# Performance work log

Measured on AMD Instinct MI355X. Metric: run time of the kernel, lower is better.

Reference implementation:

```python
import jax, jax.numpy as jnp
import numpy as np

EMBED_DIM = 1024
NUM_HEADS = 16
HEAD_DIM = EMBED_DIM // NUM_HEADS
B, N = 8, 1024


def setup_inputs() -> dict:
    key = jax.random.key(0)
    k1, k2, k3, k4, k5, k6 = jax.random.split(key, 6)
    scale = 1.0 / np.sqrt(EMBED_DIM)
    return {
        "x": jax.random.normal(k1, (B, N, EMBED_DIM), dtype=jnp.float32),
        "attn_mask": jax.random.normal(k2, (N, N), dtype=jnp.float32) * 0.1,
        "in_proj_weight": jax.random.normal(k3, (3 * EMBED_DIM, EMBED_DIM), dtype=jnp.float32) * scale,
        "in_proj_bias": jax.random.normal(k4, (3 * EMBED_DIM,), dtype=jnp.float32) * 0.02,
        "out_w": jax.random.normal(k5, (EMBED_DIM, EMBED_DIM), dtype=jnp.float32) * scale,
        "out_b": jax.random.normal(k6, (EMBED_DIM,), dtype=jnp.float32) * 0.02,
    }


def reference(x, attn_mask, in_proj_weight, in_proj_bias, out_w, out_b):
    # x: (B, N, C); fused QKV projection as in forward_direct
    Bn, Nn, C = x.shape
    H, D = NUM_HEADS, HEAD_DIM
    qkv = x @ in_proj_weight.T + in_proj_bias            # (B, N, 3C)
    qkv = qkv.reshape(Bn, Nn, 3, H, D).transpose(2, 0, 3, 1, 4)  # (3, B, H, N, D)
    q, k, v = qkv[0], qkv[1], qkv[2]
    q = q / jnp.sqrt(jnp.asarray(D, dtype=q.dtype))
    attn = jnp.einsum("bhnd,bhmd->bhnm", q, k)           # (B, H, N, N) scores
    attn = attn + attn_mask                              # broadcast over (B, H)
    attn = jax.nn.softmax(attn, axis=-1)
    out = jnp.einsum("bhnm,bhmd->bhnd", attn, v)         # (B, H, N, D)
    out = out.transpose(0, 2, 1, 3).reshape(Bn, Nn, C)   # (B, N, C)
    return out @ out_w.T + out_b
```

## Files before the change

### kernel.cpp

```cpp
#include <hip/hip_runtime.h>


typedef __bf16 bf16x8 __attribute__((ext_vector_type(8)));
typedef float f32x4 __attribute__((ext_vector_type(4)));
typedef unsigned short us4v __attribute__((ext_vector_type(4)));

#define MFMA16 __builtin_amdgcn_mfma_f32_16x16x32_bf16

__device__ __forceinline__ unsigned short f2bf(float f) {
    return __builtin_bit_cast(unsigned short, (__bf16)f);
}

__device__ __forceinline__ us4v cvt4(float4 v) {
    us4v r;
    r.x = f2bf(v.x); r.y = f2bf(v.y); r.z = f2bf(v.z); r.w = f2bf(v.w);
    return r;
}

__device__ __forceinline__ void gl16(const unsigned short* g, unsigned short* l) {
    __builtin_amdgcn_global_load_lds(
        (const __attribute__((address_space(1))) unsigned*)g,
        (__attribute__((address_space(3))) unsigned*)l, 16, 0, 0);
}

__global__ __launch_bounds__(256)
void cvt_bf16(const float* __restrict__ src, unsigned short* __restrict__ dst,
              int n4) {
    const int i = blockIdx.x * 256 + threadIdx.x;
    if (i < n4) {
        float4 v = ((const float4*)src)[i];
        ((us4v*)dst)[i] = cvt4(v);
    }
}

__global__ __launch_bounds__(256, 3)
void qkv_gemm(const unsigned short* __restrict__ xb,
              const unsigned short* __restrict__ wb,
              const float* __restrict__ bias,
              unsigned short* __restrict__ qb, unsigned short* __restrict__ kb,
              unsigned short* __restrict__ vbT)
{
    __shared__ unsigned short lsa[3][128 * 32];
    __shared__ unsigned short lsb[3][128 * 32];
    const int tid  = threadIdx.x;
    const int wave = tid >> 6, lane = tid & 63;
    const int quad = lane >> 4, l15 = lane & 15;
    const int rch = (quad ^ ((l15 >> 1) & 3)) * 8;
    const int m0 = blockIdx.x * 128, n0 = blockIdx.y * 128;
    const int wm = (wave & 1) * 64, wn = (wave >> 1) * 64;

    const int srow = wave * 32 + (lane >> 2);
    const int scol = ((lane & 3) ^ ((lane >> 3) & 3)) * 8;
    const unsigned short* ga = xb + (size_t)(m0 + srow) * 1024 + scol;
    const unsigned short* gb = wb + (size_t)(n0 + srow) * 1024 + scol;
    const int so0 = (wave * 32) * 32;
    const int so1 = (wave * 32 + 16) * 32;

    f32x4 acc[4][4];
#pragma unroll
    for (int i = 0; i < 4; ++i)
#pragma unroll
        for (int j = 0; j < 4; ++j) acc[i][j] = (f32x4){0.f, 0.f, 0.f, 0.f};

    gl16(ga, &lsa[0][so0]);
    gl16(ga + 16 * 1024, &lsa[0][so1]);
    gl16(gb, &lsb[0][so0]);
    gl16(gb + 16 * 1024, &lsb[0][so1]);
    gl16(ga + 32, &lsa[1][so0]);
    gl16(ga + 16 * 1024 + 32, &lsa[1][so1]);
    gl16(gb + 32, &lsb[1][so0]);
    gl16(gb + 16 * 1024 + 32, &lsb[1][so1]);

    for (int kt = 0; kt < 32; ++kt) {
        const int cb = kt % 3;
        if (kt < 30) {
            const int k0 = (kt + 2) * 32;
            const int sb = (kt + 2) % 3;
            gl16(ga + k0, &lsa[sb][so0]);
            gl16(ga + 16 * 1024 + k0, &lsa[sb][so1]);
            gl16(gb + k0, &lsb[sb][so0]);
            gl16(gb + 16 * 1024 + k0, &lsb[sb][so1]);
            asm volatile("s_waitcnt vmcnt(8)" ::: "memory");
        } else if (kt == 30) {
            asm volatile("s_waitcnt vmcnt(4)" ::: "memory");
        } else {
            asm volatile("s_waitcnt vmcnt(0)" ::: "memory");
        }
        __builtin_amdgcn_s_barrier();

        const unsigned short* pa = lsa[cb];
        const unsigned short* pb = lsb[cb];
        bf16x8 af[4], bfr[4];
#pragma unroll
        for (int i = 0; i < 4; ++i)
            af[i] = *(const bf16x8*)&pa[(wm + i * 16 + l15) * 32 + rch];
#pragma unroll
        for (int j = 0; j < 4; ++j)
            bfr[j] = *(const bf16x8*)&pb[(wn + j * 16 + l15) * 32 + rch];
#pragma unroll
        for (int i = 0; i < 4; ++i)
#pragma unroll
            for (int j = 0; j < 4; ++j)
                acc[i][j] = MFMA16(af[i], bfr[j], acc[i][j], 0, 0, 0);

        asm volatile("s_waitcnt lgkmcnt(0)" ::: "memory");
        __builtin_amdgcn_sched_barrier(0);
        __builtin_amdgcn_s_barrier();
    }

    const int which = n0 >> 10;
    if (which == 2) {
#pragma unroll
        for (int j = 0; j < 4; ++j) {
            const int n = n0 + wn + j * 16 + l15;
            const int c = n & 1023;
            const int h = c >> 6, d = c & 63;
            const float bv = bias[n];
#pragma unroll
            for (int i = 0; i < 4; ++i) {
                const int m = m0 + wm + i * 16 + quad * 4;
                const int b = m >> 10, s = m & 1023;
                us4v pk;
#pragma unroll
                for (int r = 0; r < 4; ++r) pk[r] = f2bf(acc[i][j][r] + bv);
                *(us4v*)&vbT[(size_t)((b * 16 + h) * 64 + d) * 1024 + s] = pk;
            }
        }
    } else {
        unsigned short* __restrict__ dst = (which == 0) ? qb : kb;
        const float sc = (which == 0) ? 0.125f : 1.0f;
#pragma unroll
        for (int j = 0; j < 4; ++j) {
            const int n = n0 + wn + j * 16 + l15;
            const int c = n & 1023;
            const int h = c >> 6, d = c & 63;
            const float bv = bias[n];
#pragma unroll
            for (int i = 0; i < 4; ++i)
#pragma unroll
                for (int r = 0; r < 4; ++r) {
                    const int m = m0 + wm + i * 16 + quad * 4 + r;
                    const int b = m >> 10, s = m & 1023;
                    const float v = (acc[i][j][r] + bv) * sc;
                    dst[(size_t)((b * 16 + h) * 1024 + s) * 64 + d] = f2bf(v);
                }
        }
    }
}

__global__ __launch_bounds__(256, 3)
void attn_kernel(const unsigned short* __restrict__ qb,
                 const unsigned short* __restrict__ kb,
                 const unsigned short* __restrict__ vbT,
                 const float* __restrict__ mask,
                 unsigned short* __restrict__ ob)
{
    __shared__ unsigned short lsk[2][2][64 * 32];
    __shared__ unsigned short lsv[2][2][64 * 32];
    __shared__ unsigned short lsp[4][2][16 * 64];
    const int tid  = threadIdx.x;
    const int wave = tid >> 6, lane = tid & 63;
    const int quad = lane >> 4, l15 = lane & 15;
    const int rch = (quad ^ ((l15 >> 1) & 3)) * 8;
    const int swz = (l15 & 7) << 3;
    const int p  = blockIdx.x;
    const int lg = (p & 7) * 128 + (p >> 3);
    const int bh = lg >> 3;
    const int q0 = (lg & 7) * 128;
    const int b = bh >> 4, h = bh & 15;

    const unsigned short* __restrict__ kbase = kb + (size_t)bh * 65536;
    const unsigned short* __restrict__ vtb  = vbT + (size_t)bh * 65536;

    const int scol = ((lane & 3) ^ ((lane >> 3) & 3)) * 8;
    const unsigned short* gk = kbase + (size_t)(wave * 16 + (lane >> 2)) * 64
                                     + scol;
    const unsigned short* gv = vtb + (size_t)(wave * 16 + (lane >> 2)) * 1024
                                   + scol;
    const int so = (wave * 16) * 32;

    bf16x8 bq[2][2];
#pragma unroll
    for (int g = 0; g < 2; ++g) {
        const unsigned short* qrow =
            qb + (size_t)(bh * 1024 + q0 + wave * 32 + g * 16 + l15) * 64;
        bq[g][0] = *(const bf16x8*)(qrow + quad * 8);
        bq[g][1] = *(const bf16x8*)(qrow + 32 + quad * 8);
    }

    float lsum[2] = {0.f, 0.f};
    f32x4 oacc[2][4];
#pragma unroll
    for (int g = 0; g < 2; ++g)
#pragma unroll
        for (int nt = 0; nt < 4; ++nt) oacc[g][nt] = (f32x4){0.f, 0.f, 0.f, 0.f};

    const float* __restrict__ mrow0 =
        mask + (size_t)(q0 + wave * 32 + l15) * 1024;
    const float* __restrict__ mrow1 = mrow0 + 16 * 1024;

    gl16(gk, &lsk[0][0][so]);
    gl16(gk + 32, &lsk[0][1][so]);
    gl16(gv, &lsv[0][0][so]);
    gl16(gv + 32, &lsv[0][1][so]);
    float4 mcur[2][4];
#pragma unroll
    for (int nt = 0; nt < 4; ++nt) {
        mcur[0][nt] = *(const float4*)&mrow0[nt * 16 + quad * 4];
        mcur[1][nt] = *(const float4*)&mrow1[nt * 16 + quad * 4];
    }
    __syncthreads();

    int buf = 0;
    for (int kt = 0; kt < 16; ++kt) {
        float4 mnext[2][4];
        if (kt < 15) {
            gl16(gk + (size_t)(kt + 1) * 4096, &lsk[buf ^ 1][0][so]);
            gl16(gk + (size_t)(kt + 1) * 4096 + 32, &lsk[buf ^ 1][1][so]);
            gl16(gv + (size_t)(kt + 1) * 64, &lsv[buf ^ 1][0][so]);
            gl16(gv + (size_t)(kt + 1) * 64 + 32, &lsv[buf ^ 1][1][so]);
            __builtin_amdgcn_sched_barrier(0);
#pragma unroll
            for (int nt = 0; nt < 4; ++nt) {
                mnext[0][nt] =
                    *(const float4*)&mrow0[(kt + 1) * 64 + nt * 16 + quad * 4];
                mnext[1][nt] =
                    *(const float4*)&mrow1[(kt + 1) * 64 + nt * 16 + quad * 4];
            }
        }

        const unsigned short* rk0 = lsk[buf][0];
        const unsigned short* rk1 = lsk[buf][1];
        f32x4 s[2][4];
        __builtin_amdgcn_s_setprio(1);
#pragma unroll
        for (int nt = 0; nt < 4; ++nt) {
            const bf16x8 k0 = *(const bf16x8*)&rk0[(nt * 16 + l15) * 32 + rch];
            const bf16x8 k1 = *(const bf16x8*)&rk1[(nt * 16 + l15) * 32 + rch];
            s[0][nt] = MFMA16(k0, bq[0][0], (f32x4){0.f, 0.f, 0.f, 0.f}, 0, 0, 0);
            s[0][nt] = MFMA16(k1, bq[0][1], s[0][nt], 0, 0, 0);
            s[1][nt] = MFMA16(k0, bq[1][0], (f32x4){0.f, 0.f, 0.f, 0.f}, 0, 0, 0);
            s[1][nt] = MFMA16(k1, bq[1][1], s[1][nt], 0, 0, 0);
        }
        __builtin_amdgcn_s_setprio(0);

        unsigned short* lp0 = lsp[wave][0];
        unsigned short* lp1 = lsp[wave][1];
#pragma unroll
        for (int nt = 0; nt < 4; ++nt) {
            us4v pk0, pk1;
#pragma unroll
            for (int r = 0; r < 4; ++r) {
                const float pe0 =
                    __expf(s[0][nt][r] + ((const float*)&mcur[0][nt])[r]);
                const float pe1 =
                    __expf(s[1][nt][r] + ((const float*)&mcur[1][nt])[r]);
                lsum[0] += pe0;
                lsum[1] += pe1;
                pk0[r] = f2bf(pe0);
                pk1[r] = f2bf(pe1);
            }
            const int off = (nt * 16 + quad * 4) ^ swz;
            *(us4v*)&lp0[(l15 << 6) + off] = pk0;
            *(us4v*)&lp1[(l15 << 6) + off] = pk1;
        }
        bf16x8 pb0[2], pb1[2];
        pb0[0] = *(const bf16x8*)&lp0[(l15 << 6) + ((quad * 8) ^ swz)];
        pb0[1] = *(const bf16x8*)&lp0[(l15 << 6) + ((32 + quad * 8) ^ swz)];
        pb1[0] = *(const bf16x8*)&lp1[(l15 << 6) + ((quad * 8) ^ swz)];
        pb1[1] = *(const bf16x8*)&lp1[(l15 << 6) + ((32 + quad * 8) ^ swz)];

        const unsigned short* rv0 = lsv[buf][0];
        const unsigned short* rv1 = lsv[buf][1];
        __builtin_amdgcn_s_setprio(1);
#pragma unroll
        for (int nt = 0; nt < 4; ++nt) {
            const bf16x8 v0 = *(const bf16x8*)&rv0[(nt * 16 + l15) * 32 + rch];
            const bf16x8 v1 = *(const bf16x8*)&rv1[(nt * 16 + l15) * 32 + rch];
            oacc[0][nt] = MFMA16(v0, pb0[0], oacc[0][nt], 0, 0, 0);
            oacc[0][nt] = MFMA16(v1, pb0[1], oacc[0][nt], 0, 0, 0);
            oacc[1][nt] = MFMA16(v0, pb1[0], oacc[1][nt], 0, 0, 0);
            oacc[1][nt] = MFMA16(v1, pb1[1], oacc[1][nt], 0, 0, 0);
        }
        __builtin_amdgcn_s_setprio(0);

        if (kt < 15) {
            asm volatile("s_waitcnt lgkmcnt(0)" ::: "memory");
            __builtin_amdgcn_sched_barrier(0);
            asm volatile("s_waitcnt vmcnt(8)" ::: "memory");
            __builtin_amdgcn_s_barrier();
#pragma unroll
            for (int g = 0; g < 2; ++g)
#pragma unroll
                for (int nt = 0; nt < 4; ++nt) mcur[g][nt] = mnext[g][nt];
        }
        buf ^= 1;
    }

#pragma unroll
    for (int g = 0; g < 2; ++g) {
        lsum[g] += __shfl_xor(lsum[g], 16, 64);
        lsum[g] += __shfl_xor(lsum[g], 32, 64);
    }
#pragma unroll
    for (int g = 0; g < 2; ++g) {
        const float inv = 1.0f / lsum[g];
        unsigned short* orow =
            ob + (size_t)(b * 1024 + q0 + wave * 32 + g * 16 + l15) * 1024
               + h * 64;
#pragma unroll
        for (int nt = 0; nt < 4; ++nt) {
            us4v o;
#pragma unroll
            for (int r = 0; r < 4; ++r) o[r] = f2bf(oacc[g][nt][r] * inv);
            *(us4v*)&orow[nt * 16 + quad * 4] = o;
        }
    }
}

__global__ __launch_bounds__(256, 3)
void out_gemm(const unsigned short* __restrict__ a,
              const unsigned short* __restrict__ wb,
              const float* __restrict__ bias, float* __restrict__ out)
{
    __shared__ unsigned short lsa[3][128 * 32];
    __shared__ unsigned short lsb[3][128 * 32];
    const int tid  = threadIdx.x;
    const int wave = tid >> 6, lane = tid & 63;
    const int quad = lane >> 4, l15 = lane & 15;
    const int rch = (quad ^ ((l15 >> 1) & 3)) * 8;
    const int m0 = blockIdx.x * 128, n0 = blockIdx.y * 128;
    const int wm = (wave & 1) * 64, wn = (wave >> 1) * 64;

    const int srow = wave * 32 + (lane >> 2);
    const int scol = ((lane & 3) ^ ((lane >> 3) & 3)) * 8;
    const unsigned short* ga = a + (size_t)(m0 + srow) * 1024 + scol;
    const unsigned short* gb = wb + (size_t)(n0 + srow) * 1024 + scol;
    const int so0 = (wave * 32) * 32;
    const int so1 = (wave * 32 + 16) * 32;

    f32x4 acc[4][4];
#pragma unroll
    for (int i = 0; i < 4; ++i)
#pragma unroll
        for (int j = 0; j < 4; ++j) acc[i][j] = (f32x4){0.f, 0.f, 0.f, 0.f};

    gl16(ga, &lsa[0][so0]);
    gl16(ga + 16 * 1024, &lsa[0][so1]);
    gl16(gb, &lsb[0][so0]);
    gl16(gb + 16 * 1024, &lsb[0][so1]);
    gl16(ga + 32, &lsa[1][so0]);
    gl16(ga + 16 * 1024 + 32, &lsa[1][so1]);
    gl16(gb + 32, &lsb[1][so0]);
    gl16(gb + 16 * 1024 + 32, &lsb[1][so1]);

    for (int kt = 0; kt < 32; ++kt) {
        const int cb = kt % 3;
        if (kt < 30) {
            const int k0 = (kt + 2) * 32;
            const int sb = (kt + 2) % 3;
            gl16(ga + k0, &lsa[sb][so0]);
            gl16(ga + 16 * 1024 + k0, &lsa[sb][so1]);
            gl16(gb + k0, &lsb[sb][so0]);
            gl16(gb + 16 * 1024 + k0, &lsb[sb][so1]);
            asm volatile("s_waitcnt vmcnt(8)" ::: "memory");
        } else if (kt == 30) {
            asm volatile("s_waitcnt vmcnt(4)" ::: "memory");
        } else {
            asm volatile("s_waitcnt vmcnt(0)" ::: "memory");
        }
        __builtin_amdgcn_s_barrier();

        const unsigned short* pa = lsa[cb];
        const unsigned short* pb = lsb[cb];
        bf16x8 af[4], bfr[4];
#pragma unroll
        for (int i = 0; i < 4; ++i)
            af[i] = *(const bf16x8*)&pa[(wm + i * 16 + l15) * 32 + rch];
#pragma unroll
        for (int j = 0; j < 4; ++j)
            bfr[j] = *(const bf16x8*)&pb[(wn + j * 16 + l15) * 32 + rch];
#pragma unroll
        for (int i = 0; i < 4; ++i)
#pragma unroll
            for (int j = 0; j < 4; ++j)
                acc[i][j] = MFMA16(af[i], bfr[j], acc[i][j], 0, 0, 0);

        asm volatile("s_waitcnt lgkmcnt(0)" ::: "memory");
        __builtin_amdgcn_sched_barrier(0);
        __builtin_amdgcn_s_barrier();
    }

#pragma unroll
    for (int j = 0; j < 4; ++j) {
        const int n = n0 + wn + j * 16 + l15;
        const float bv = bias[n];
#pragma unroll
        for (int i = 0; i < 4; ++i)
#pragma unroll
            for (int r = 0; r < 4; ++r) {
                const int m = m0 + wm + i * 16 + quad * 4 + r;
                out[(size_t)m * 1024 + n] = acc[i][j][r] + bv;
            }
    }
}

extern "C" void kernel_launch(void* const* d_in, const int* in_sizes, int n_in,
                              void* d_out, int out_size, void* d_ws, size_t ws_size,
                              hipStream_t stream) {
    const float* x    = (const float*)d_in[0];
    const float* mask = (const float*)d_in[1];
    const float* win  = (const float*)d_in[2];
    const float* bin  = (const float*)d_in[3];
    const float* wout = (const float*)d_in[4];
    const float* bout = (const float*)d_in[5];
    float* out = (float*)d_out;

    char* ws = (char*)d_ws;
    unsigned short* xb = (unsigned short*)(ws);
    unsigned short* ob = (unsigned short*)(ws);
    unsigned short* qb = (unsigned short*)(ws + (size_t)(16 << 20));
    unsigned short* kb = (unsigned short*)(ws + (size_t)(32 << 20));
    unsigned short* vbT = (unsigned short*)(ws + (size_t)(48 << 20));
    unsigned short* winb  = (unsigned short*)d_out;
    unsigned short* woutb = qb;

    cvt_bf16<<<dim3(8192), 256, 0, stream>>>(x, xb, 8 * 1024 * 1024 / 4);
    cvt_bf16<<<dim3(3072), 256, 0, stream>>>(win, winb, 3 * 1024 * 1024 / 4);
    qkv_gemm<<<dim3(64, 24), 256, 0, stream>>>(xb, winb, bin, qb, kb, vbT);
    attn_kernel<<<dim3(1024), 256, 0, stream>>>(qb, kb, vbT, mask, ob);
    cvt_bf16<<<dim3(1024), 256, 0, stream>>>(wout, woutb, 1024 * 1024 / 4);
    out_gemm<<<dim3(64, 8), 256, 0, stream>>>(ob, woutb, bout, out);
}
```

Before: 277.3 us.

## Load K/V fragments directly from global memory, dropping LDS staging and barriers

The attention kernel stops staging K and V tiles in shared memory through double-buffered global_load_lds with block barriers. Each wave now loads its own K and V MFMA fragments straight from global memory into registers every iteration, and the mask prefetch pipeline is removed. This cuts LDS use and all block-level synchronisation, which may raise occupancy. In exchange, every wave re-reads the same K/V data through the cache, and there is no software prefetch to hide global load latency.

```diff
diff --git a/kernel.cpp b/kernel.cpp
--- a/kernel.cpp
+++ b/kernel.cpp
@@ -155,13 +155,10 @@
                  const float* __restrict__ mask,
                  unsigned short* __restrict__ ob)
 {
-    __shared__ unsigned short lsk[2][2][64 * 32];
-    __shared__ unsigned short lsv[2][2][64 * 32];
     __shared__ unsigned short lsp[4][2][16 * 64];
     const int tid  = threadIdx.x;
     const int wave = tid >> 6, lane = tid & 63;
     const int quad = lane >> 4, l15 = lane & 15;
-    const int rch = (quad ^ ((l15 >> 1) & 3)) * 8;
     const int swz = (l15 & 7) << 3;
     const int p  = blockIdx.x;
     const int lg = (p & 7) * 128 + (p >> 3);
@@ -169,15 +166,10 @@
     const int q0 = (lg & 7) * 128;
     const int b = bh >> 4, h = bh & 15;
 
-    const unsigned short* __restrict__ kbase = kb + (size_t)bh * 65536;
-    const unsigned short* __restrict__ vtb  = vbT + (size_t)bh * 65536;
-
-    const int scol = ((lane & 3) ^ ((lane >> 3) & 3)) * 8;
-    const unsigned short* gk = kbase + (size_t)(wave * 16 + (lane >> 2)) * 64
-                                     + scol;
-    const unsigned short* gv = vtb + (size_t)(wave * 16 + (lane >> 2)) * 1024
-                                   + scol;
-    const int so = (wave * 16) * 32;
+    const unsigned short* gk =
+        kb + (size_t)bh * 65536 + (size_t)l15 * 64 + quad * 8;
+    const unsigned short* gv =
+        vbT + (size_t)bh * 65536 + (size_t)l15 * 1024 + quad * 8;
 
     bf16x8 bq[2][2];
 #pragma unroll
@@ -198,63 +190,53 @@
     const float* __restrict__ mrow0 =
         mask + (size_t)(q0 + wave * 32 + l15) * 1024;
     const float* __restrict__ mrow1 = mrow0 + 16 * 1024;
-
-    gl16(gk, &lsk[0][0][so]);
-    gl16(gk + 32, &lsk[0][1][so]);
-    gl16(gv, &lsv[0][0][so]);
-    gl16(gv + 32, &lsv[0][1][so]);
-    float4 mcur[2][4];
-#pragma unroll
-    for (int nt = 0; nt < 4; ++nt) {
-        mcur[0][nt] = *(const float4*)&mrow0[nt * 16 + quad * 4];
-        mcur[1][nt] = *(const float4*)&mrow1[nt * 16 + quad * 4];
-    }
-    __syncthreads();
-
-    int buf = 0;
+    unsigned short* lp0 = lsp[wave][0];
+    unsigned short* lp1 = lsp[wave][1];
+
     for (int kt = 0; kt < 16; ++kt) {
-        float4 mnext[2][4];
-        if (kt < 15) {
-            gl16(gk + (size_t)(kt + 1) * 4096, &lsk[buf ^ 1][0][so]);
-            gl16(gk + (size_t)(kt + 1) * 4096 + 32, &lsk[buf ^ 1][1][so]);
-            gl16(gv + (size_t)(kt + 1) * 64, &lsv[buf ^ 1][0][so]);
-            gl16(gv + (size_t)(kt + 1) * 64 + 32, &lsv[buf ^ 1][1][so]);
-            __builtin_amdgcn_sched_barrier(0);
-#pragma unroll
-            for (int nt = 0; nt < 4; ++nt) {
-                mnext[0][nt] =
-                    *(const float4*)&mrow0[(kt + 1) * 64 + nt * 16 + quad * 4];
-                mnext[1][nt] =
-                    *(const float4*)&mrow1[(kt + 1) * 64 + nt * 16 + quad * 4];
-            }
-        }
-
-        const unsigned short* rk0 = lsk[buf][0];
-        const unsigned short* rk1 = lsk[buf][1];
+        bf16x8 kf[4][2];
+#pragma unroll
+        for (int nt = 0; nt < 4; ++nt) {
+            const unsigned short* kr = gk + (size_t)(kt * 64 + nt * 16) * 64;
+            kf[nt][0] = *(const bf16x8*)(kr);
+            kf[nt][1] = *(const bf16x8*)(kr + 32);
+        }
+        float4 mv[2][4];
+#pragma unroll
+        for (int nt = 0; nt < 4; ++nt) {
+            mv[0][nt] = *(const float4*)&mrow0[kt * 64 + nt * 16 + quad * 4];
+            mv[1][nt] = *(const float4*)&mrow1[kt * 64 + nt * 16 + quad * 4];
+        }
+        bf16x8 vf[4][2];
+#pragma unroll
+        for (int nt = 0; nt < 4; ++nt) {
+            const unsigned short* vr = gv + (size_t)nt * 16 * 1024 + kt * 64;
+            vf[nt][0] = *(const bf16x8*)(vr);
+            vf[nt][1] = *(const bf16x8*)(vr + 32);
+        }
+
         f32x4 s[2][4];
         __builtin_amdgcn_s_setprio(1);
 #pragma unroll
         for (int nt = 0; nt < 4; ++nt) {
-            const bf16x8 k0 = *(const bf16x8*)&rk0[(nt * 16 + l15) * 32 + rch];
-            const bf16x8 k1 = *(const bf16x8*)&rk1[(nt * 16 + l15) * 32 + rch];
-            s[0][nt] = MFMA16(k0, bq[0][0], (f32x4){0.f, 0.f, 0.f, 0.f}, 0, 0, 0);
-            s[0][nt] = MFMA16(k1, bq[0][1], s[0][nt], 0, 0, 0);
-            s[1][nt] = MFMA16(k0, bq[1][0], (f32x4){0.f, 0.f, 0.f, 0.f}, 0, 0, 0);
-            s[1][nt] = MFMA16(k1, bq[1][1], s[1][nt], 0, 0, 0);
+            s[0][nt] = MFMA16(kf[nt][0], bq[0][0],
+                              (f32x4){0.f, 0.f, 0.f, 0.f}, 0, 0, 0);
+            s[0][nt] = MFMA16(kf[nt][1], bq[0][1], s[0][nt], 0, 0, 0);
+            s[1][nt] = MFMA16(kf[nt][0], bq[1][0],
+                              (f32x4){0.f, 0.f, 0.f, 0.f}, 0, 0, 0);
+            s[1][nt] = MFMA16(kf[nt][1], bq[1][1], s[1][nt], 0, 0, 0);
         }
         __builtin_amdgcn_s_setprio(0);
 
-        unsigned short* lp0 = lsp[wave][0];
-        unsigned short* lp1 = lsp[wave][1];
 #pragma unroll
         for (int nt = 0; nt < 4; ++nt) {
             us4v pk0, pk1;
 #pragma unroll
             for (int r = 0; r < 4; ++r) {
                 const float pe0 =
-                    __expf(s[0][nt][r] + ((const float*)&mcur[0][nt])[r]);
+                    __expf(s[0][nt][r] + ((const float*)&mv[0][nt])[r]);
                 const float pe1 =
-                    __expf(s[1][nt][r] + ((const float*)&mcur[1][nt])[r]);
+                    __expf(s[1][nt][r] + ((const float*)&mv[1][nt])[r]);
                 lsum[0] += pe0;
                 lsum[1] += pe1;
                 pk0[r] = f2bf(pe0);
@@ -270,31 +252,15 @@
         pb1[0] = *(const bf16x8*)&lp1[(l15 << 6) + ((quad * 8) ^ swz)];
         pb1[1] = *(const bf16x8*)&lp1[(l15 << 6) + ((32 + quad * 8) ^ swz)];
 
-        const unsigned short* rv0 = lsv[buf][0];
-        const unsigned short* rv1 = lsv[buf][1];
         __builtin_amdgcn_s_setprio(1);
 #pragma unroll
         for (int nt = 0; nt < 4; ++nt) {
-            const bf16x8 v0 = *(const bf16x8*)&rv0[(nt * 16 + l15) * 32 + rch];
-            const bf16x8 v1 = *(const bf16x8*)&rv1[(nt * 16 + l15) * 32 + rch];
-            oacc[0][nt] = MFMA16(v0, pb0[0], oacc[0][nt], 0, 0, 0);
-            oacc[0][nt] = MFMA16(v1, pb0[1], oacc[0][nt], 0, 0, 0);
-            oacc[1][nt] = MFMA16(v0, pb1[0], oacc[1][nt], 0, 0, 0);
-            oacc[1][nt] = MFMA16(v1, pb1[1], oacc[1][nt], 0, 0, 0);
+            oacc[0][nt] = MFMA16(vf[nt][0], pb0[0], oacc[0][nt], 0, 0, 0);
+            oacc[0][nt] = MFMA16(vf[nt][1], pb0[1], oacc[0][nt], 0, 0, 0);
+            oacc[1][nt] = MFMA16(vf[nt][0], pb1[0], oacc[1][nt], 0, 0, 0);
+            oacc[1][nt] = MFMA16(vf[nt][1], pb1[1], oacc[1][nt], 0, 0, 0);
         }
         __builtin_amdgcn_s_setprio(0);
-
-        if (kt < 15) {
-            asm volatile("s_waitcnt lgkmcnt(0)" ::: "memory");
-            __builtin_amdgcn_sched_barrier(0);
-            asm volatile("s_waitcnt vmcnt(8)" ::: "memory");
-            __builtin_amdgcn_s_barrier();
-#pragma unroll
-            for (int g = 0; g < 2; ++g)
-#pragma unroll
-                for (int nt = 0; nt < 4; ++nt) mcur[g][nt] = mnext[g][nt];
-        }
-        buf ^= 1;
     }
 
 #pragma unroll
```

Measured after the change: 363.8 us. +31.2%, slower.

## Rewrite attention with 32x32 MFMA, register-resident P, and exp2 softmax

Applied to the files above, without the earlier changes.

Rebuilds the attention inner loop around 32x32x16 bf16 MFMA so each wave owns 32 query rows. The probability tile is repacked in registers with cvt_pk_bf16 and permlane32_swap, which removes the LDS round-trip for P. Q and the mask are pre-scaled by log2(e) so exp2 replaces expf, and the mask is loaded straight into the MFMA accumulator as its initial value. This adds a small mask-scaling kernel and a full __syncthreads per tile, and drops the cross-iteration mask prefetch, so mask load latency is less hidden.

```diff
diff --git a/kernel.cpp b/kernel.cpp
--- a/kernel.cpp
+++ b/kernel.cpp
@@ -3,9 +3,12 @@
 
 typedef __bf16 bf16x8 __attribute__((ext_vector_type(8)));
 typedef float f32x4 __attribute__((ext_vector_type(4)));
+typedef float f32x16 __attribute__((ext_vector_type(16)));
 typedef unsigned short us4v __attribute__((ext_vector_type(4)));
+typedef unsigned int u32x4 __attribute__((ext_vector_type(4)));
 
 #define MFMA16 __builtin_amdgcn_mfma_f32_16x16x32_bf16
+#define MFMA32 __builtin_amdgcn_mfma_f32_32x32x16_bf16
 
 __device__ __forceinline__ unsigned short f2bf(float f) {
     return __builtin_bit_cast(unsigned short, (__bf16)f);
@@ -14,6 +17,12 @@
 __device__ __forceinline__ us4v cvt4(float4 v) {
     us4v r;
     r.x = f2bf(v.x); r.y = f2bf(v.y); r.z = f2bf(v.z); r.w = f2bf(v.w);
+    return r;
+}
+
+__device__ __forceinline__ unsigned cvtpk(float lo, float hi) {
+    unsigned r;
+    asm volatile("v_cvt_pk_bf16_f32 %0, %1, %2" : "=v"(r) : "v"(lo), "v"(hi));
     return r;
 }
 
@@ -30,6 +39,17 @@
     if (i < n4) {
         float4 v = ((const float4*)src)[i];
         ((us4v*)dst)[i] = cvt4(v);
+    }
+}
+
+__global__ __launch_bounds__(256)
+void scale_f32(const float* __restrict__ src, float* __restrict__ dst, int n4) {
+    const int i = blockIdx.x * 256 + threadIdx.x;
+    if (i < n4) {
+        float4 v = ((const float4*)src)[i];
+        const float s = 1.4426950408889634f;
+        v.x *= s; v.y *= s; v.z *= s; v.w *= s;
+        ((float4*)dst)[i] = v;
     }
 }
 
@@ -128,7 +148,7 @@
         }
     } else {
         unsigned short* __restrict__ dst = (which == 0) ? qb : kb;
-        const float sc = (which == 0) ? 0.125f : 1.0f;
+        const float sc = (which == 0) ? 0.18033688011112442f : 1.0f;
 #pragma unroll
         for (int j = 0; j < 4; ++j) {
             const int n = n0 + wn + j * 16 + l15;
@@ -152,170 +172,152 @@
 void attn_kernel(const unsigned short* __restrict__ qb,
                  const unsigned short* __restrict__ kb,
                  const unsigned short* __restrict__ vbT,
-                 const float* __restrict__ mask,
+                 const float* __restrict__ mask2,
                  unsigned short* __restrict__ ob)
 {
     __shared__ unsigned short lsk[2][2][64 * 32];
     __shared__ unsigned short lsv[2][2][64 * 32];
-    __shared__ unsigned short lsp[4][2][16 * 64];
     const int tid  = threadIdx.x;
     const int wave = tid >> 6, lane = tid & 63;
-    const int quad = lane >> 4, l15 = lane & 15;
-    const int rch = (quad ^ ((l15 >> 1) & 3)) * 8;
-    const int swz = (l15 & 7) << 3;
+    const int r5 = lane & 31, hl = lane >> 5;
+    const int rs = ((r5 >> 1) ^ (r5 >> 3)) & 3;
     const int p  = blockIdx.x;
     const int lg = (p & 7) * 128 + (p >> 3);
     const int bh = lg >> 3;
     const int q0 = (lg & 7) * 128;
-    const int b = bh >> 4, h = bh & 15;
+    const int b = bh >> 4, head = bh & 15;
 
     const unsigned short* __restrict__ kbase = kb + (size_t)bh * 65536;
     const unsigned short* __restrict__ vtb  = vbT + (size_t)bh * 65536;
 
-    const int scol = ((lane & 3) ^ ((lane >> 3) & 3)) * 8;
+    const int scol =
+        ((lane & 3) ^ ((lane >> 3) & 3) ^ ((2 * wave + (lane >> 5)) & 3)) * 8;
     const unsigned short* gk = kbase + (size_t)(wave * 16 + (lane >> 2)) * 64
                                      + scol;
     const unsigned short* gv = vtb + (size_t)(wave * 16 + (lane >> 2)) * 1024
                                    + scol;
     const int so = (wave * 16) * 32;
 
-    bf16x8 bq[2][2];
-#pragma unroll
-    for (int g = 0; g < 2; ++g) {
-        const unsigned short* qrow =
-            qb + (size_t)(bh * 1024 + q0 + wave * 32 + g * 16 + l15) * 64;
-        bq[g][0] = *(const bf16x8*)(qrow + quad * 8);
-        bq[g][1] = *(const bf16x8*)(qrow + 32 + quad * 8);
-    }
-
-    float lsum[2] = {0.f, 0.f};
-    f32x4 oacc[2][4];
-#pragma unroll
-    for (int g = 0; g < 2; ++g)
-#pragma unroll
-        for (int nt = 0; nt < 4; ++nt) oacc[g][nt] = (f32x4){0.f, 0.f, 0.f, 0.f};
-
-    const float* __restrict__ mrow0 =
-        mask + (size_t)(q0 + wave * 32 + l15) * 1024;
-    const float* __restrict__ mrow1 = mrow0 + 16 * 1024;
+    const int q = q0 + wave * 32 + r5;
+    bf16x8 bq[4];
+    {
+        const unsigned short* qrow = qb + (size_t)(bh * 1024 + q) * 64;
+#pragma unroll
+        for (int kk = 0; kk < 4; ++kk)
+            bq[kk] = *(const bf16x8*)(qrow + kk * 16 + hl * 8);
+    }
+
+    float lsum = 0.f;
+    f32x16 acc[2];
+#pragma unroll
+    for (int dt = 0; dt < 2; ++dt)
+#pragma unroll
+        for (int r = 0; r < 16; ++r) acc[dt][r] = 0.f;
+
+    const float* __restrict__ mq = mask2 + (size_t)q * 1024;
 
     gl16(gk, &lsk[0][0][so]);
     gl16(gk + 32, &lsk[0][1][so]);
     gl16(gv, &lsv[0][0][so]);
     gl16(gv + 32, &lsv[0][1][so]);
-    float4 mcur[2][4];
-#pragma unroll
-    for (int nt = 0; nt < 4; ++nt) {
-        mcur[0][nt] = *(const float4*)&mrow0[nt * 16 + quad * 4];
-        mcur[1][nt] = *(const float4*)&mrow1[nt * 16 + quad * 4];
-    }
     __syncthreads();
 
     int buf = 0;
     for (int kt = 0; kt < 16; ++kt) {
-        float4 mnext[2][4];
+        f32x16 msk[2];
+#pragma unroll
+        for (int t32 = 0; t32 < 2; ++t32)
+#pragma unroll
+            for (int oct = 0; oct < 4; ++oct) {
+                const float4 mv = *(const float4*)
+                    &mq[kt * 64 + t32 * 32 + oct * 8 + hl * 4];
+                msk[t32][4 * oct + 0] = mv.x;
+                msk[t32][4 * oct + 1] = mv.y;
+                msk[t32][4 * oct + 2] = mv.z;
+                msk[t32][4 * oct + 3] = mv.w;
+            }
+        __builtin_amdgcn_sched_barrier(0);
         if (kt < 15) {
             gl16(gk + (size_t)(kt + 1) * 4096, &lsk[buf ^ 1][0][so]);
             gl16(gk + (size_t)(kt + 1) * 4096 + 32, &lsk[buf ^ 1][1][so]);
             gl16(gv + (size_t)(kt + 1) * 64, &lsv[buf ^ 1][0][so]);
             gl16(gv + (size_t)(kt + 1) * 64 + 32, &lsv[buf ^ 1][1][so]);
-            __builtin_amdgcn_sched_barrier(0);
-#pragma unroll
-            for (int nt = 0; nt < 4; ++nt) {
-                mnext[0][nt] =
-                    *(const float4*)&mrow0[(kt + 1) * 64 + nt * 16 + quad * 4];
-                mnext[1][nt] =
-                    *(const float4*)&mrow1[(kt + 1) * 64 + nt * 16 + quad * 4];
-            }
-        }
-
-        const unsigned short* rk0 = lsk[buf][0];
-        const unsigned short* rk1 = lsk[buf][1];
-        f32x4 s[2][4];
-        __builtin_amdgcn_s_setprio(1);
-#pragma unroll
-        for (int nt = 0; nt < 4; ++nt) {
-            const bf16x8 k0 = *(const bf16x8*)&rk0[(nt * 16 + l15) * 32 + rch];
-            const bf16x8 k1 = *(const bf16x8*)&rk1[(nt * 16 + l15) * 32 + rch];
-            s[0][nt] = MFMA16(k0, bq[0][0], (f32x4){0.f, 0.f, 0.f, 0.f}, 0, 0, 0);
-            s[0][nt] = MFMA16(k1, bq[0][1], s[0][nt], 0, 0, 0);
-            s[1][nt] = MFMA16(k0, bq[1][0], (f32x4){0.f, 0.f, 0.f, 0.f}, 0, 0, 0);
-            s[1][nt] = MFMA16(k1, bq[1][1], s[1][nt], 0, 0, 0);
-        }
-        __builtin_amdgcn_s_setprio(0);
-
-        unsigned short* lp0 = lsp[wave][0];
-        unsigned short* lp1 = lsp[wave][1];
-#pragma unroll
-        for (int nt = 0; nt < 4; ++nt) {
-            us4v pk0, pk1;
-#pragma unroll
-            for (int r = 0; r < 4; ++r) {
-                const float pe0 =
-                    __expf(s[0][nt][r] + ((const float*)&mcur[0][nt])[r]);
-                const float pe1 =
-                    __expf(s[1][nt][r] + ((const float*)&mcur[1][nt])[r]);
-                lsum[0] += pe0;
-                lsum[1] += pe1;
-                pk0[r] = f2bf(pe0);
-                pk1[r] = f2bf(pe1);
-            }
-            const int off = (nt * 16 + quad * 4) ^ swz;
-            *(us4v*)&lp0[(l15 << 6) + off] = pk0;
-            *(us4v*)&lp1[(l15 << 6) + off] = pk1;
-        }
-        bf16x8 pb0[2], pb1[2];
-        pb0[0] = *(const bf16x8*)&lp0[(l15 << 6) + ((quad * 8) ^ swz)];
-        pb0[1] = *(const bf16x8*)&lp0[(l15 << 6) + ((32 + quad * 8) ^ swz)];
-        pb1[0] = *(const bf16x8*)&lp1[(l15 << 6) + ((quad * 8) ^ swz)];
-        pb1[1] = *(const bf16x8*)&lp1[(l15 << 6) + ((32 + quad * 8) ^ swz)];
-
-        const unsigned short* rv0 = lsv[buf][0];
-        const unsigned short* rv1 = lsv[buf][1];
-        __builtin_amdgcn_s_setprio(1);
-#pragma unroll
-        for (int nt = 0; nt < 4; ++nt) {
-            const bf16x8 v0 = *(const bf16x8*)&rv0[(nt * 16 + l15) * 32 + rch];
-            const bf16x8 v1 = *(const bf16x8*)&rv1[(nt * 16 + l15) * 32 + rch];
-            oacc[0][nt] = MFMA16(v0, pb0[0], oacc[0][nt], 0, 0, 0);
-            oacc[0][nt] = MFMA16(v1, pb0[1], oacc[0][nt], 0, 0, 0);
-            oacc[1][nt] = MFMA16(v0, pb1[0], oacc[1][nt], 0, 0, 0);
-            oacc[1][nt] = MFMA16(v1, pb1[1], oacc[1][nt], 0, 0, 0);
-        }
-        __builtin_amdgcn_s_setprio(0);
-
-        if (kt < 15) {
-            asm volatile("s_waitcnt lgkmcnt(0)" ::: "memory");
-            __builtin_amdgcn_sched_barrier(0);
-            asm volatile("s_waitcnt vmcnt(8)" ::: "memory");
-            __builtin_amdgcn_s_barrier();
-#pragma unroll
-            for (int g = 0; g < 2; ++g)
-#pragma unroll
-                for (int nt = 0; nt < 4; ++nt) mcur[g][nt] = mnext[g][nt];
-        }
+        }
+
+#pragma unroll
+        for (int t32 = 0; t32 < 2; ++t32) {
+            f32x16 s = msk[t32];
+            __builtin_amdgcn_s_setprio(1);
+#pragma unroll
+            for (int kk = 0; kk < 4; ++kk) {
+                const unsigned short* kp = lsk[buf][kk >> 1];
+                const int c4 = 2 * (kk & 1) + hl;
+                const bf16x8 ka = *(const bf16x8*)
+                    &kp[(t32 * 32 + r5) * 32 + ((c4 ^ rs) * 8)];
+                s = MFMA32(ka, bq[kk], s, 0, 0, 0);
+            }
+            __builtin_amdgcn_s_setprio(0);
+
+            float pv[16];
+            float ts = 0.f;
+#pragma unroll
+            for (int r = 0; r < 16; ++r) {
+                pv[r] = exp2f(s[r]);
+                ts += pv[r];
+            }
+            lsum += ts;
+
+            bf16x8 pfr[2];
+#pragma unroll
+            for (int cl = 0; cl < 2; ++cl) {
+                unsigned xa = cvtpk(pv[8 * cl + 0], pv[8 * cl + 1]);
+                unsigned xb = cvtpk(pv[8 * cl + 2], pv[8 * cl + 3]);
+                unsigned ya = cvtpk(pv[8 * cl + 4], pv[8 * cl + 5]);
+                unsigned yb = cvtpk(pv[8 * cl + 6], pv[8 * cl + 7]);
+                asm volatile("v_permlane32_swap_b32 %0, %1"
+                             : "+v"(xa), "+v"(ya));
+                asm volatile("v_permlane32_swap_b32 %0, %1"
+                             : "+v"(xb), "+v"(yb));
+                const u32x4 t = {xa, xb, ya, yb};
+                pfr[cl] = __builtin_bit_cast(bf16x8, t);
+            }
+
+            __builtin_amdgcn_s_setprio(1);
+#pragma unroll
+            for (int cl = 0; cl < 2; ++cl) {
+                const int cg = t32 * 2 + cl;
+                const unsigned short* vp = lsv[buf][cg >> 1];
+                const int c4v = 2 * (cg & 1) + hl;
+                const int voff = (c4v ^ rs) * 8;
+#pragma unroll
+                for (int dt = 0; dt < 2; ++dt) {
+                    const bf16x8 va = *(const bf16x8*)
+                        &vp[(dt * 32 + r5) * 32 + voff];
+                    acc[dt] = MFMA32(va, pfr[cl], acc[dt], 0, 0, 0);
+                }
+            }
+            __builtin_amdgcn_s_setprio(0);
+        }
+
+        __syncthreads();
         buf ^= 1;
     }
 
-#pragma unroll
-    for (int g = 0; g < 2; ++g) {
-        lsum[g] += __shfl_xor(lsum[g], 16, 64);
-        lsum[g] += __shfl_xor(lsum[g], 32, 64);
-    }
-#pragma unroll
-    for (int g = 0; g < 2; ++g) {
-        const float inv = 1.0f / lsum[g];
-        unsigned short* orow =
-            ob + (size_t)(b * 1024 + q0 + wave * 32 + g * 16 + l15) * 1024
-               + h * 64;
-#pragma unroll
-        for (int nt = 0; nt < 4; ++nt) {
+    lsum += __shfl_xor(lsum, 32, 64);
+    const float inv = 1.0f / lsum;
+
+    unsigned short* orow =
+        ob + (size_t)(b * 1024 + q) * 1024 + head * 64;
+#pragma unroll
+    for (int dt = 0; dt < 2; ++dt)
+#pragma unroll
+        for (int oct = 0; oct < 4; ++oct) {
             us4v o;
 #pragma unroll
-            for (int r = 0; r < 4; ++r) o[r] = f2bf(oacc[g][nt][r] * inv);
-            *(us4v*)&orow[nt * 16 + quad * 4] = o;
-        }
-    }
+            for (int r = 0; r < 4; ++r)
+                o[r] = f2bf(acc[dt][4 * oct + r] * inv);
+            *(us4v*)&orow[dt * 32 + oct * 8 + hl * 4] = o;
+        }
 }
 
 __global__ __launch_bounds__(256, 3)
@@ -423,12 +425,14 @@
     unsigned short* kb = (unsigned short*)(ws + (size_t)(32 << 20));
     unsigned short* vbT = (unsigned short*)(ws + (size_t)(48 << 20));
     unsigned short* winb  = (unsigned short*)d_out;
+    float* mask2 = (float*)((char*)d_out + (size_t)(6 << 20));
     unsigned short* woutb = qb;
 
     cvt_bf16<<<dim3(8192), 256, 0, stream>>>(x, xb, 8 * 1024 * 1024 / 4);
     cvt_bf16<<<dim3(3072), 256, 0, stream>>>(win, winb, 3 * 1024 * 1024 / 4);
+    scale_f32<<<dim3(1024), 256, 0, stream>>>(mask, mask2, 1024 * 1024 / 4);
     qkv_gemm<<<dim3(64, 24), 256, 0, stream>>>(xb, winb, bin, qb, kb, vbT);
-    attn_kernel<<<dim3(1024), 256, 0, stream>>>(qb, kb, vbT, mask, ob);
+    attn_kernel<<<dim3(1024), 256, 0, stream>>>(qb, kb, vbT, mask2, ob);
     cvt_bf16<<<dim3(1024), 256, 0, stream>>>(wout, woutb, 1024 * 1024 / 4);
     out_gemm<<<dim3(64, 8), 256, 0, stream>>>(ob, woutb, bout, out);
 }
```

New measurement: 280.2 us. About the same (+1.0%).
